# Optimization experiments

Hardware: AMD Instinct MI355X
Metric: run time of the kernel (lower is better)

Reference implementation:

```python
import jax, jax.numpy as jnp
import numpy as np

H = 16       # num_heads
FD = 16      # feature_dim
HD = 64      # head_dim = hidden // num_kv_heads
EPS = 1e-5   # attention normalization eps
LN_EPS = 1e-5


def setup_inputs() -> dict:
    key = jax.random.key(0)
    ks = jax.random.split(key, 5)
    b, l, hid = 2, 2048, 1024
    x = jax.random.normal(ks[0], (b, l, hid), dtype=jnp.float32)
    Wq = jax.random.normal(ks[1], (H * FD, hid), dtype=jnp.float32) * 0.02
    Wk = jax.random.normal(ks[2], (H * FD, hid), dtype=jnp.float32) * 0.02
    Wv = jax.random.normal(ks[3], (hid, hid), dtype=jnp.float32) * 0.02
    Wo = jax.random.normal(ks[4], (hid, hid), dtype=jnp.float32) * 0.02
    gamma = jnp.ones((FD,), dtype=jnp.float32)
    beta = jnp.zeros((FD,), dtype=jnp.float32)
    return {"x": x, "Wq": Wq, "Wk": Wk, "Wv": Wv, "Wo": Wo, "gamma": gamma, "beta": beta}


def _feature_map(t, gamma, beta):
    # RebasedFeatureMap without flatten: layer_norm (no affine) -> *gamma + beta
    mu = jnp.mean(t, axis=-1, keepdims=True)
    var = jnp.mean(jnp.square(t - mu), axis=-1, keepdims=True)
    t = (t - mu) * jax.lax.rsqrt(var + LN_EPS)
    return t * gamma + beta


def reference(x, Wq, Wk, Wv, Wo, gamma, beta):
    b, l, hid = x.shape
    # projections -> (b, h, l, d)
    q = (x @ Wq.T).reshape(b, l, H, FD).transpose(0, 2, 1, 3)
    k = (x @ Wk.T).reshape(b, l, H, FD).transpose(0, 2, 1, 3)
    v = (x @ Wv.T).reshape(b, l, H, HD).transpose(0, 2, 1, 3)
    q = _feature_map(q, gamma, beta) * (FD ** -0.5)  # use_scale=True in parallel_rebased
    k = _feature_map(k, gamma, beta)
    # phi(q).phi(k) with squared feature map == (q.k)^2
    s = jnp.square(jnp.einsum('bhid,bhjd->bhij', q, k))
    mask = jnp.tril(jnp.ones((l, l), dtype=bool))  # causal
    s = jnp.where(mask, s, jnp.float32(0))
    o = jnp.einsum('bhij,bhjd->bhid', s, v)
    z = jnp.sum(s, axis=-1, keepdims=True) + EPS    # use_normalize=True
    o = o / z
    o = o.transpose(0, 2, 1, 3).reshape(b, l, H * HD)
    return o @ Wo.T
```

## Files before the change

### kernel.cpp

```cpp
#include <hip/hip_runtime.h>
#include <cstddef>
#include <cstdint>


typedef __attribute__((ext_vector_type(8)))  __bf16 bf16x8;
typedef __attribute__((ext_vector_type(4)))  __bf16 bf16x4;
typedef __attribute__((ext_vector_type(4)))  float  f32x4;
typedef __attribute__((ext_vector_type(8)))  unsigned short ushort8;
typedef __attribute__((ext_vector_type(4)))  unsigned short ushort4v;

__device__ __forceinline__ unsigned short f2b(float f) {
    union { float f; unsigned u; } v; v.f = f;
    unsigned r = v.u + 0x7FFFu + ((v.u >> 16) & 1u);
    return (unsigned short)(r >> 16);
}
__device__ __forceinline__ float b2f(unsigned short b) {
    union { unsigned u; float f; } v; v.u = ((unsigned)b) << 16;
    return v.f;
}

typedef const __attribute__((address_space(1))) void* gas_ptr;
typedef __attribute__((address_space(3))) void* las_ptr;

__device__ __forceinline__ void gload_lds16(const unsigned short* g, unsigned short* l) {
    __builtin_amdgcn_global_load_lds((gas_ptr)g, (las_ptr)l, 16, 0, 0);
}

template <int BM, int BN, int OUTMODE>
__global__ __launch_bounds__(256) void gemm_mfma(const unsigned short* __restrict__ A,
                                                 const unsigned short* __restrict__ W,
                                                 void* __restrict__ Cout,
                                                 int M, int N, int K) {
    constexpr int BK = 64;
    constexpr int MF = BM / 32;
    constexpr int NF = BN / 32;
    __shared__ __align__(16) unsigned short As[BM * BK];
    __shared__ __align__(16) unsigned short Bs[BN * BK];

    const int t = threadIdx.x;
    const int wid = t >> 6, lane = t & 63;
    const int m0 = blockIdx.x * BM, n0 = blockIdx.y * BN;
    const int wrow = (wid >> 1) * (BM / 2);
    const int wcol = (wid & 1) * (BN / 2);
    const int lr = lane & 15, lk = (lane >> 4) * 8;

    f32x4 acc[MF][NF];
#pragma unroll
    for (int m = 0; m < MF; ++m)
#pragma unroll
        for (int n = 0; n < NF; ++n) acc[m][n] = (f32x4){0.f, 0.f, 0.f, 0.f};

    const unsigned short* Ag = A + (size_t)m0 * K;
    const unsigned short* Wg = W + (size_t)n0 * K;

    for (int k0 = 0; k0 < K; k0 += BK) {
        __syncthreads();
#pragma unroll
        for (int i = 0; i < BM / 32; ++i) {
            const int e = (i * 256 + wid * 64 + lane) * 8;
            gload_lds16(Ag + (size_t)(e >> 6) * K + k0 + (e & 63),
                        As + (size_t)(i * 256 + wid * 64) * 8);
        }
#pragma unroll
        for (int i = 0; i < BN / 32; ++i) {
            const int e = (i * 256 + wid * 64 + lane) * 8;
            gload_lds16(Wg + (size_t)(e >> 6) * K + k0 + (e & 63),
                        Bs + (size_t)(i * 256 + wid * 64) * 8);
        }
        __syncthreads();

#pragma unroll
        for (int kk = 0; kk < BK; kk += 32) {
            bf16x8 af[MF], bf[NF];
#pragma unroll
            for (int m = 0; m < MF; ++m)
                af[m] = *(const bf16x8*)&As[(wrow + m * 16 + lr) * BK + kk + lk];
#pragma unroll
            for (int n = 0; n < NF; ++n)
                bf[n] = *(const bf16x8*)&Bs[(wcol + n * 16 + lr) * BK + kk + lk];
#pragma unroll
            for (int m = 0; m < MF; ++m)
#pragma unroll
                for (int n = 0; n < NF; ++n)
                    acc[m][n] = __builtin_amdgcn_mfma_f32_16x16x32_bf16(af[m], bf[n], acc[m][n], 0, 0, 0);
        }
    }

    const int orow0 = m0 + wrow + (lane >> 4) * 4;
    const int ocol0 = n0 + wcol + lr;
#pragma unroll
    for (int m = 0; m < MF; ++m)
#pragma unroll
        for (int n = 0; n < NF; ++n) {
            if (OUTMODE == 2) {
                const int nc = ocol0 + n * 16;
                const int mrow = orow0 + m * 16;
                unsigned short* dst = (unsigned short*)Cout
                    + (size_t)((mrow >> 11) * 16 + (nc >> 6)) * (64 * 2048)
                    + (size_t)(nc & 63) * 2048 + (mrow & 2047);
                ushort4v pv;
#pragma unroll
                for (int i = 0; i < 4; ++i) pv[i] = f2b(acc[m][n][i]);
                *(ushort4v*)dst = pv;
            } else {
#pragma unroll
                for (int i = 0; i < 4; ++i) {
                    const size_t idx = (size_t)(orow0 + m * 16 + i) * N + ocol0 + n * 16;
                    if (OUTMODE == 1) ((unsigned short*)Cout)[idx] = f2b(acc[m][n][i]);
                    else              ((float*)Cout)[idx] = acc[m][n][i];
                }
            }
        }
}

__global__ __launch_bounds__(256) void gemm_split(const unsigned short* __restrict__ Ah,
                                                  const unsigned short* __restrict__ Al,
                                                  const unsigned short* __restrict__ Wh,
                                                  const unsigned short* __restrict__ Wl,
                                                  float* __restrict__ C,
                                                  int M, int N, int K) {
    constexpr int BM = 64, BN = 64, BK = 64;
    constexpr int MF = 2, NF = 2;
    __shared__ __align__(16) unsigned short Ahs[BM * BK];
    __shared__ __align__(16) unsigned short Als[BM * BK];
    __shared__ __align__(16) unsigned short Bhs[BN * BK];
    __shared__ __align__(16) unsigned short Bls[BN * BK];

    const int t = threadIdx.x;
    const int wid = t >> 6, lane = t & 63;
    const int m0 = blockIdx.x * BM, n0 = blockIdx.y * BN;
    const int wrow = (wid >> 1) * 32;
    const int wcol = (wid & 1) * 32;
    const int lr = lane & 15, lk = (lane >> 4) * 8;

    f32x4 acc[MF][NF];
#pragma unroll
    for (int m = 0; m < MF; ++m)
#pragma unroll
        for (int n = 0; n < NF; ++n) acc[m][n] = (f32x4){0.f, 0.f, 0.f, 0.f};

    const unsigned short* Ahg = Ah + (size_t)m0 * K;
    const unsigned short* Alg = Al + (size_t)m0 * K;
    const unsigned short* Whg = Wh + (size_t)n0 * K;
    const unsigned short* Wlg = Wl + (size_t)n0 * K;

    for (int k0 = 0; k0 < K; k0 += BK) {
        __syncthreads();
#pragma unroll
        for (int i = 0; i < BM / 32; ++i) {
            const int e = (i * 256 + wid * 64 + lane) * 8;
            const size_t go = (size_t)(e >> 6) * K + k0 + (e & 63);
            const size_t lo = (size_t)(i * 256 + wid * 64) * 8;
            gload_lds16(Ahg + go, Ahs + lo);
            gload_lds16(Alg + go, Als + lo);
            gload_lds16(Whg + go, Bhs + lo);
            gload_lds16(Wlg + go, Bls + lo);
        }
        __syncthreads();

#pragma unroll
        for (int kk = 0; kk < BK; kk += 32) {
            bf16x8 afh[MF], afl[MF], bfh[NF], bfl[NF];
#pragma unroll
            for (int m = 0; m < MF; ++m) {
                afh[m] = *(const bf16x8*)&Ahs[(wrow + m * 16 + lr) * BK + kk + lk];
                afl[m] = *(const bf16x8*)&Als[(wrow + m * 16 + lr) * BK + kk + lk];
            }
#pragma unroll
            for (int n = 0; n < NF; ++n) {
                bfh[n] = *(const bf16x8*)&Bhs[(wcol + n * 16 + lr) * BK + kk + lk];
                bfl[n] = *(const bf16x8*)&Bls[(wcol + n * 16 + lr) * BK + kk + lk];
            }
#pragma unroll
            for (int m = 0; m < MF; ++m)
#pragma unroll
                for (int n = 0; n < NF; ++n) {
                    acc[m][n] = __builtin_amdgcn_mfma_f32_16x16x32_bf16(afh[m], bfh[n], acc[m][n], 0, 0, 0);
                    acc[m][n] = __builtin_amdgcn_mfma_f32_16x16x32_bf16(afh[m], bfl[n], acc[m][n], 0, 0, 0);
                    acc[m][n] = __builtin_amdgcn_mfma_f32_16x16x32_bf16(afl[m], bfh[n], acc[m][n], 0, 0, 0);
                }
        }
    }

    const int orow0 = m0 + wrow + (lane >> 4) * 4;
    const int ocol0 = n0 + wcol + lr;
#pragma unroll
    for (int m = 0; m < MF; ++m)
#pragma unroll
        for (int n = 0; n < NF; ++n)
#pragma unroll
            for (int i = 0; i < 4; ++i)
                C[(size_t)(orow0 + m * 16 + i) * N + ocol0 + n * 16] = acc[m][n][i];
}

__global__ __launch_bounds__(256) void cast_bf16(const float* __restrict__ in,
                                                 unsigned short* __restrict__ out, int n) {
    const int i = (blockIdx.x * 256 + threadIdx.x) * 8;
    if (i >= n) return;
    float4 a = *(const float4*)(in + i);
    float4 b = *(const float4*)(in + i + 4);
    ushort8 o;
    o[0] = f2b(a.x); o[1] = f2b(a.y); o[2] = f2b(a.z); o[3] = f2b(a.w);
    o[4] = f2b(b.x); o[5] = f2b(b.y); o[6] = f2b(b.z); o[7] = f2b(b.w);
    *(ushort8*)(out + i) = o;
}

__global__ __launch_bounds__(256) void cast_split(const float* __restrict__ in,
                                                  unsigned short* __restrict__ hi,
                                                  unsigned short* __restrict__ lo, int n) {
    const int i = (blockIdx.x * 256 + threadIdx.x) * 8;
    if (i >= n) return;
    float4 a = *(const float4*)(in + i);
    float4 b = *(const float4*)(in + i + 4);
    float xv[8] = {a.x, a.y, a.z, a.w, b.x, b.y, b.z, b.w};
    ushort8 oh, ol;
#pragma unroll
    for (int e = 0; e < 8; ++e) {
        const unsigned short h = f2b(xv[e]);
        oh[e] = h;
        ol[e] = f2b(xv[e] - b2f(h));
    }
    *(ushort8*)(hi + i) = oh;
    *(ushort8*)(lo + i) = ol;
}

__global__ __launch_bounds__(256) void ln_featuremap(const float* __restrict__ qk,
                                                     const float* __restrict__ gamma,
                                                     const float* __restrict__ beta,
                                                     unsigned short* __restrict__ qhl,
                                                     unsigned short* __restrict__ khl) {
    const int gid = blockIdx.x * 256 + threadIdx.x;
    const int idx = gid & 31;
    const int m = gid >> 5;
    const int b = m >> 11, l = m & 2047;
    const int h = idx & 15;
    const float scale = (idx < 16) ? 0.25f : 1.0f;
    const float* p = qk + (size_t)gid * 16;

    float xv[16];
    float4 v0 = *(const float4*)(p + 0);
    float4 v1 = *(const float4*)(p + 4);
    float4 v2 = *(const float4*)(p + 8);
    float4 v3 = *(const float4*)(p + 12);
    xv[0]=v0.x; xv[1]=v0.y; xv[2]=v0.z; xv[3]=v0.w;
    xv[4]=v1.x; xv[5]=v1.y; xv[6]=v1.z; xv[7]=v1.w;
    xv[8]=v2.x; xv[9]=v2.y; xv[10]=v2.z; xv[11]=v2.w;
    xv[12]=v3.x; xv[13]=v3.y; xv[14]=v3.z; xv[15]=v3.w;

    float mu = 0.f;
#pragma unroll
    for (int f = 0; f < 16; ++f) mu += xv[f];
    mu *= 0.0625f;
    float var = 0.f;
#pragma unroll
    for (int f = 0; f < 16; ++f) { float d = xv[f] - mu; var = fmaf(d, d, var); }
    var *= 0.0625f;
    const float rs = rsqrtf(var + 1e-5f);

    ushort8 hi0, hi1, lo0, lo1;
#pragma unroll
    for (int f = 0; f < 16; ++f) {
        const float v = ((xv[f] - mu) * rs * gamma[f] + beta[f]) * scale;
        const unsigned short hb = f2b(v);
        const unsigned short lb = f2b(v - b2f(hb));
        if (f < 8) { hi0[f] = hb; lo0[f] = lb; }
        else       { hi1[f - 8] = hb; lo1[f - 8] = lb; }
    }
    unsigned short* dst = ((idx < 16) ? qhl : khl)
        + ((size_t)(b * 16 + h) * 2048 + l) * 32;
    *(ushort8*)(dst + 0)  = hi0;
    *(ushort8*)(dst + 8)  = hi1;
    *(ushort8*)(dst + 16) = lo0;
    *(ushort8*)(dst + 24) = lo1;
}

__global__ __launch_bounds__(256) void rebased_attn(const unsigned short* __restrict__ qhl_g,
                                                    const unsigned short* __restrict__ khl_g,
                                                    const unsigned short* __restrict__ vT,
                                                    unsigned short* __restrict__ o) {
    const int bh = blockIdx.y;
    const int bb = bh >> 4;
    const int t = threadIdx.x;
    const int wid = t >> 6, lane = t & 63;
    const int fr = lane & 15;
    const int fg = lane >> 4;

    __shared__ __align__(16) unsigned short qhl[4 * 64 * 8];
    __shared__ __align__(16) unsigned short khl[2][4 * 64 * 8];
    __shared__ __align__(16) unsigned short vsl[2][8 * 64 * 8];
    __shared__ __align__(16) __bf16 P[64][72];

    const unsigned short* qg  = qhl_g + (size_t)bh * 2048 * 32;
    const unsigned short* kg  = khl_g + (size_t)bh * 2048 * 32;
    const unsigned short* vbh = vT + (size_t)bh * 64 * 2048;
    unsigned short*       obh = o  + (size_t)bb * 2048 * 1024 + (bh & 15) * 64;

    const bf16x8 z8 = {(__bf16)0.f,(__bf16)0.f,(__bf16)0.f,(__bf16)0.f,
                       (__bf16)0.f,(__bf16)0.f,(__bf16)0.f,(__bf16)0.f};
    const f32x4 zc = (f32x4){0.f, 0.f, 0.f, 0.f};

    for (int pass = 0; pass < 2; ++pass) {
        const int qt = pass ? (31 - (int)blockIdx.x) : (int)blockIdx.x;
        const int qbase = qt << 6;

        __syncthreads();
        gload_lds16(qg + (size_t)(qbase + lane) * 32 + wid * 8, qhl + wid * 512);
        gload_lds16(kg + (size_t)lane * 32 + wid * 8, &khl[0][wid * 512]);
        gload_lds16(vbh + (size_t)lane * 2048 + (2 * wid) * 8, &vsl[0][(2 * wid) * 512]);
        gload_lds16(vbh + (size_t)lane * 2048 + (2 * wid + 1) * 8, &vsl[0][(2 * wid + 1) * 512]);
        __syncthreads();

        const bf16x8 bq1 = *(const bf16x8*)&qhl[(((fg & 1)    ) * 64 + 16 * wid + fr) * 8];
        const bf16x8 bq2 = *(const bf16x8*)&qhl[(((fg & 1) + 2) * 64 + 16 * wid + fr) * 8];

        f32x4 oacc[4];
#pragma unroll
        for (int n = 0; n < 4; ++n) oacc[n] = zc;
        float zlane = 0.f;

        int cur = 0;
        for (int kt = 0; kt <= qt; ++kt) {
            if (kt < qt) {
                const int nb = cur ^ 1;
                gload_lds16(kg + (size_t)(((kt + 1) << 6) + lane) * 32 + wid * 8,
                            &khl[nb][wid * 512]);
                gload_lds16(vbh + (size_t)lane * 2048 + ((kt + 1) << 6) + (2 * wid) * 8,
                            &vsl[nb][(2 * wid) * 512]);
                gload_lds16(vbh + (size_t)lane * 2048 + ((kt + 1) << 6) + (2 * wid + 1) * 8,
                            &vsl[nb][(2 * wid + 1) * 512]);
            }

#pragma unroll
            for (int nrow = 0; nrow < 4; ++nrow) {
                const bf16x8 ak  = *(const bf16x8*)&khl[cur][(fg * 64 + nrow * 16 + fr) * 8];
                const bf16x8 ak2 = (fg < 2) ? ak : z8;
                f32x4 s = __builtin_amdgcn_mfma_f32_16x16x32_bf16(ak2, bq2, zc, 0, 0, 0);
                s = __builtin_amdgcn_mfma_f32_16x16x32_bf16(ak, bq1, s, 0, 0, 0);

                float s2[4];
                if (kt == qt) {
                    const int qr = 16 * wid + fr;
                    const int kc = nrow * 16 + fg * 4;
#pragma unroll
                    for (int reg = 0; reg < 4; ++reg) {
                        float x = s[reg];
                        float y = x * x;
                        s2[reg] = (kc + reg <= qr) ? y : 0.f;
                        zlane += s2[reg];
                    }
                } else {
#pragma unroll
                    for (int reg = 0; reg < 4; ++reg) {
                        float x = s[reg];
                        s2[reg] = x * x;
                        zlane += s2[reg];
                    }
                }
                bf16x4 pv = {(__bf16)s2[0], (__bf16)s2[1], (__bf16)s2[2], (__bf16)s2[3]};
                *(bf16x4*)&P[16 * wid + fr][nrow * 16 + fg * 4] = pv;
            }

            const bf16x8 a0 = *(const bf16x8*)&P[16 * wid + fr][fg * 8];
            const bf16x8 a1 = *(const bf16x8*)&P[16 * wid + fr][32 + fg * 8];
#pragma unroll
            for (int nt = 0; nt < 4; ++nt) {
                const bf16x8 b0 = *(const bf16x8*)&vsl[cur][((fg    ) * 64 + nt * 16 + fr) * 8];
                const bf16x8 b1 = *(const bf16x8*)&vsl[cur][((fg + 4) * 64 + nt * 16 + fr) * 8];
                oacc[nt] = __builtin_amdgcn_mfma_f32_16x16x32_bf16(a0, b0, oacc[nt], 0, 0, 0);
                oacc[nt] = __builtin_amdgcn_mfma_f32_16x16x32_bf16(a1, b1, oacc[nt], 0, 0, 0);
            }

            asm volatile("s_waitcnt vmcnt(0)" ::: "memory");
            __builtin_amdgcn_s_barrier();
            cur ^= 1;
        }

        float z = zlane;
        z += __shfl_xor(z, 16);
        z += __shfl_xor(z, 32);
        const float zinv = 1.f / (z + 1e-5f);

#pragma unroll
        for (int reg = 0; reg < 4; ++reg) {
            const float r = __shfl(zinv, fg * 4 + reg);
            const size_t gro = (size_t)(qbase + 16 * wid + fg * 4 + reg) * 1024;
#pragma unroll
            for (int nt = 0; nt < 4; ++nt)
                obh[gro + nt * 16 + fr] = f2b(oacc[nt][reg] * r);
        }
    }
}

extern "C" void kernel_launch(void* const* d_in, const int* in_sizes, int n_in,
                              void* d_out, int out_size, void* d_ws, size_t ws_size,
                              hipStream_t stream) {
    const float* x     = (const float*)d_in[0];
    const float* Wq    = (const float*)d_in[1];
    const float* Wk    = (const float*)d_in[2];
    const float* Wv    = (const float*)d_in[3];
    const float* Wo    = (const float*)d_in[4];
    const float* gamma = (const float*)d_in[5];
    const float* beta  = (const float*)d_in[6];
    float* out = (float*)d_out;
    (void)in_sizes; (void)n_in; (void)out_size; (void)ws_size;

    char* w = (char*)d_ws;
    float*          qk_raw = (float*)w;
    unsigned short* vTb    = (unsigned short*)(w + (8u  << 20));
    unsigned short* ob     = (unsigned short*)(w + (16u << 20));
    unsigned short* xh     = (unsigned short*)(w + (24u << 20));
    unsigned short* xl     = (unsigned short*)(w + (32u << 20));
    unsigned short* qhl_g  = (unsigned short*)(w + (24u << 20));
    unsigned short* khl_g  = (unsigned short*)(w + (28u << 20));
    unsigned short* wqkh   = (unsigned short*)(w + (40u << 20));
    unsigned short* wqkl   = (unsigned short*)(w + (41u << 20));
    unsigned short* wvb    = (unsigned short*)(w + (42u << 20));
    unsigned short* wob    = (unsigned short*)(w + (44u << 20));

    cast_split<<<2048, 256, 0, stream>>>(x,  xh, xl, 4096 * 1024);
    cast_split<<<128,  256, 0, stream>>>(Wq, wqkh, wqkl, 256 * 1024);
    cast_split<<<128,  256, 0, stream>>>(Wk, wqkh + 256 * 1024, wqkl + 256 * 1024, 256 * 1024);
    cast_bf16 <<<512,  256, 0, stream>>>(Wv, wvb, 1024 * 1024);
    cast_bf16 <<<512,  256, 0, stream>>>(Wo, wob, 1024 * 1024);

    gemm_split<<<dim3(64, 8), 256, 0, stream>>>(xh, xl, wqkh, wqkl, qk_raw, 4096, 512, 1024);
    gemm_mfma<64, 128, 2><<<dim3(64, 8), 256, 0, stream>>>(xh, wvb, vTb, 4096, 1024, 1024);
    ln_featuremap<<<512, 256, 0, stream>>>(qk_raw, gamma, beta, qhl_g, khl_g);
    rebased_attn<<<dim3(16, 32), 256, 0, stream>>>(qhl_g, khl_g, vTb, ob);
    gemm_mfma<64, 128, 0><<<dim3(64, 8), 256, 0, stream>>>(ob, wob, out, 4096, 1024, 1024);
}
```

Before: 125.3 us.

## Use one query tile per block with triple-buffered KV prefetch and smaller GEMM tiles

The attention kernel no longer pairs query tiles i and 31-i inside one block. It launches 32 query tiles per head, each handled by its own block, and loads the Q fragments straight from global memory into registers. K/V staging goes from double to triple buffering, with a partial vmcnt wait so two tiles can be in flight while one is computed. The V-projection and output GEMMs switch to 64x64 tiles with twice the grid. These changes aim to raise occupancy and overlap memory latency. In exchange the causal work per block becomes unbalanced and each block uses more LDS.

```diff
diff --git a/kernel.cpp b/kernel.cpp
--- a/kernel.cpp
+++ b/kernel.cpp
@@ -284,10 +284,11 @@
     const int wid = t >> 6, lane = t & 63;
     const int fr = lane & 15;
     const int fg = lane >> 4;
-
-    __shared__ __align__(16) unsigned short qhl[4 * 64 * 8];
-    __shared__ __align__(16) unsigned short khl[2][4 * 64 * 8];
-    __shared__ __align__(16) unsigned short vsl[2][8 * 64 * 8];
+    const int qt = blockIdx.x;
+    const int qbase = qt << 6;
+
+    __shared__ __align__(16) unsigned short khl[3][4 * 64 * 8];
+    __shared__ __align__(16) unsigned short vsl[3][8 * 64 * 8];
     __shared__ __align__(16) __bf16 P[64][72];
 
     const unsigned short* qg  = qhl_g + (size_t)bh * 2048 * 32;
@@ -299,95 +300,93 @@
                        (__bf16)0.f,(__bf16)0.f,(__bf16)0.f,(__bf16)0.f};
     const f32x4 zc = (f32x4){0.f, 0.f, 0.f, 0.f};
 
-    for (int pass = 0; pass < 2; ++pass) {
-        const int qt = pass ? (31 - (int)blockIdx.x) : (int)blockIdx.x;
-        const int qbase = qt << 6;
-
-        __syncthreads();
-        gload_lds16(qg + (size_t)(qbase + lane) * 32 + wid * 8, qhl + wid * 512);
-        gload_lds16(kg + (size_t)lane * 32 + wid * 8, &khl[0][wid * 512]);
-        gload_lds16(vbh + (size_t)lane * 2048 + (2 * wid) * 8, &vsl[0][(2 * wid) * 512]);
-        gload_lds16(vbh + (size_t)lane * 2048 + (2 * wid + 1) * 8, &vsl[0][(2 * wid + 1) * 512]);
-        __syncthreads();
-
-        const bf16x8 bq1 = *(const bf16x8*)&qhl[(((fg & 1)    ) * 64 + 16 * wid + fr) * 8];
-        const bf16x8 bq2 = *(const bf16x8*)&qhl[(((fg & 1) + 2) * 64 + 16 * wid + fr) * 8];
-
-        f32x4 oacc[4];
-#pragma unroll
-        for (int n = 0; n < 4; ++n) oacc[n] = zc;
-        float zlane = 0.f;
-
-        int cur = 0;
-        for (int kt = 0; kt <= qt; ++kt) {
-            if (kt < qt) {
-                const int nb = cur ^ 1;
-                gload_lds16(kg + (size_t)(((kt + 1) << 6) + lane) * 32 + wid * 8,
-                            &khl[nb][wid * 512]);
-                gload_lds16(vbh + (size_t)lane * 2048 + ((kt + 1) << 6) + (2 * wid) * 8,
-                            &vsl[nb][(2 * wid) * 512]);
-                gload_lds16(vbh + (size_t)lane * 2048 + ((kt + 1) << 6) + (2 * wid + 1) * 8,
-                            &vsl[nb][(2 * wid + 1) * 512]);
+    const unsigned short* qrow = qg + (size_t)(qbase + 16 * wid + fr) * 32;
+    const bf16x8 bq1 = *(const bf16x8*)&qrow[(fg & 1) * 8];
+    const bf16x8 bq2 = *(const bf16x8*)&qrow[((fg & 1) + 2) * 8];
+
+#define STAGE_KV(kt_, buf_)                                                          \
+    do {                                                                             \
+        gload_lds16(kg + ((size_t)((kt_) << 6) + lane) * 32 + wid * 8,               \
+                    &khl[buf_][wid * 512]);                                          \
+        gload_lds16(vbh + (size_t)lane * 2048 + ((kt_) << 6) + (2 * wid) * 8,        \
+                    &vsl[buf_][(2 * wid) * 512]);                                    \
+        gload_lds16(vbh + (size_t)lane * 2048 + ((kt_) << 6) + (2 * wid + 1) * 8,    \
+                    &vsl[buf_][(2 * wid + 1) * 512]);                                \
+    } while (0)
+
+    STAGE_KV(0, 0);
+    if (qt >= 1) STAGE_KV(1, 1);
+    asm volatile("s_waitcnt vmcnt(0)" ::: "memory");
+    __syncthreads();
+
+    f32x4 oacc[4];
+#pragma unroll
+    for (int n = 0; n < 4; ++n) oacc[n] = zc;
+    float zlane = 0.f;
+
+    for (int kt = 0; kt <= qt; ++kt) {
+        const int cur = kt % 3;
+        if (kt + 2 <= qt) STAGE_KV(kt + 2, (kt + 2) % 3);
+
+#pragma unroll
+        for (int nrow = 0; nrow < 4; ++nrow) {
+            const bf16x8 ak  = *(const bf16x8*)&khl[cur][(fg * 64 + nrow * 16 + fr) * 8];
+            const bf16x8 ak2 = (fg < 2) ? ak : z8;
+            f32x4 s = __builtin_amdgcn_mfma_f32_16x16x32_bf16(ak2, bq2, zc, 0, 0, 0);
+            s = __builtin_amdgcn_mfma_f32_16x16x32_bf16(ak, bq1, s, 0, 0, 0);
+
+            float s2[4];
+            if (kt == qt) {
+                const int qr = 16 * wid + fr;
+                const int kc = nrow * 16 + fg * 4;
+#pragma unroll
+                for (int reg = 0; reg < 4; ++reg) {
+                    float x = s[reg];
+                    float y = x * x;
+                    s2[reg] = (kc + reg <= qr) ? y : 0.f;
+                    zlane += s2[reg];
+                }
+            } else {
+#pragma unroll
+                for (int reg = 0; reg < 4; ++reg) {
+                    float x = s[reg];
+                    s2[reg] = x * x;
+                    zlane += s2[reg];
+                }
             }
-
-#pragma unroll
-            for (int nrow = 0; nrow < 4; ++nrow) {
-                const bf16x8 ak  = *(const bf16x8*)&khl[cur][(fg * 64 + nrow * 16 + fr) * 8];
-                const bf16x8 ak2 = (fg < 2) ? ak : z8;
-                f32x4 s = __builtin_amdgcn_mfma_f32_16x16x32_bf16(ak2, bq2, zc, 0, 0, 0);
-                s = __builtin_amdgcn_mfma_f32_16x16x32_bf16(ak, bq1, s, 0, 0, 0);
-
-                float s2[4];
-                if (kt == qt) {
-                    const int qr = 16 * wid + fr;
-                    const int kc = nrow * 16 + fg * 4;
-#pragma unroll
-                    for (int reg = 0; reg < 4; ++reg) {
-                        float x = s[reg];
-                        float y = x * x;
-                        s2[reg] = (kc + reg <= qr) ? y : 0.f;
-                        zlane += s2[reg];
-                    }
-                } else {
-#pragma unroll
-                    for (int reg = 0; reg < 4; ++reg) {
-                        float x = s[reg];
-                        s2[reg] = x * x;
-                        zlane += s2[reg];
-                    }
-                }
-                bf16x4 pv = {(__bf16)s2[0], (__bf16)s2[1], (__bf16)s2[2], (__bf16)s2[3]};
-                *(bf16x4*)&P[16 * wid + fr][nrow * 16 + fg * 4] = pv;
-            }
-
-            const bf16x8 a0 = *(const bf16x8*)&P[16 * wid + fr][fg * 8];
-            const bf16x8 a1 = *(const bf16x8*)&P[16 * wid + fr][32 + fg * 8];
-#pragma unroll
-            for (int nt = 0; nt < 4; ++nt) {
-                const bf16x8 b0 = *(const bf16x8*)&vsl[cur][((fg    ) * 64 + nt * 16 + fr) * 8];
-                const bf16x8 b1 = *(const bf16x8*)&vsl[cur][((fg + 4) * 64 + nt * 16 + fr) * 8];
-                oacc[nt] = __builtin_amdgcn_mfma_f32_16x16x32_bf16(a0, b0, oacc[nt], 0, 0, 0);
-                oacc[nt] = __builtin_amdgcn_mfma_f32_16x16x32_bf16(a1, b1, oacc[nt], 0, 0, 0);
-            }
-
-            asm volatile("s_waitcnt vmcnt(0)" ::: "memory");
-            __builtin_amdgcn_s_barrier();
-            cur ^= 1;
-        }
-
-        float z = zlane;
-        z += __shfl_xor(z, 16);
-        z += __shfl_xor(z, 32);
-        const float zinv = 1.f / (z + 1e-5f);
-
-#pragma unroll
-        for (int reg = 0; reg < 4; ++reg) {
-            const float r = __shfl(zinv, fg * 4 + reg);
-            const size_t gro = (size_t)(qbase + 16 * wid + fg * 4 + reg) * 1024;
-#pragma unroll
-            for (int nt = 0; nt < 4; ++nt)
-                obh[gro + nt * 16 + fr] = f2b(oacc[nt][reg] * r);
-        }
+            bf16x4 pv = {(__bf16)s2[0], (__bf16)s2[1], (__bf16)s2[2], (__bf16)s2[3]};
+            *(bf16x4*)&P[16 * wid + fr][nrow * 16 + fg * 4] = pv;
+        }
+
+        const bf16x8 a0 = *(const bf16x8*)&P[16 * wid + fr][fg * 8];
+        const bf16x8 a1 = *(const bf16x8*)&P[16 * wid + fr][32 + fg * 8];
+#pragma unroll
+        for (int nt = 0; nt < 4; ++nt) {
+            const bf16x8 b0 = *(const bf16x8*)&vsl[cur][((fg    ) * 64 + nt * 16 + fr) * 8];
+            const bf16x8 b1 = *(const bf16x8*)&vsl[cur][((fg + 4) * 64 + nt * 16 + fr) * 8];
+            oacc[nt] = __builtin_amdgcn_mfma_f32_16x16x32_bf16(a0, b0, oacc[nt], 0, 0, 0);
+            oacc[nt] = __builtin_amdgcn_mfma_f32_16x16x32_bf16(a1, b1, oacc[nt], 0, 0, 0);
+        }
+
+        if (kt + 2 <= qt) asm volatile("s_waitcnt vmcnt(3)" ::: "memory");
+        else              asm volatile("s_waitcnt vmcnt(0)" ::: "memory");
+        __builtin_amdgcn_s_barrier();
+        __builtin_amdgcn_sched_barrier(0);
+    }
+#undef STAGE_KV
+
+    float z = zlane;
+    z += __shfl_xor(z, 16);
+    z += __shfl_xor(z, 32);
+    const float zinv = 1.f / (z + 1e-5f);
+
+#pragma unroll
+    for (int reg = 0; reg < 4; ++reg) {
+        const float r = __shfl(zinv, fg * 4 + reg);
+        const size_t gro = (size_t)(qbase + 16 * wid + fg * 4 + reg) * 1024;
+#pragma unroll
+        for (int nt = 0; nt < 4; ++nt)
+            obh[gro + nt * 16 + fr] = f2b(oacc[nt][reg] * r);
     }
 }
 
@@ -424,8 +423,8 @@
     cast_bf16 <<<512,  256, 0, stream>>>(Wo, wob, 1024 * 1024);
 
     gemm_split<<<dim3(64, 8), 256, 0, stream>>>(xh, xl, wqkh, wqkl, qk_raw, 4096, 512, 1024);
-    gemm_mfma<64, 128, 2><<<dim3(64, 8), 256, 0, stream>>>(xh, wvb, vTb, 4096, 1024, 1024);
+    gemm_mfma<64, 64, 2><<<dim3(64, 16), 256, 0, stream>>>(xh, wvb, vTb, 4096, 1024, 1024);
     ln_featuremap<<<512, 256, 0, stream>>>(qk_raw, gamma, beta, qhl_g, khl_g);
-    rebased_attn<<<dim3(16, 32), 256, 0, stream>>>(qhl_g, khl_g, vTb, ob);
-    gemm_mfma<64, 128, 0><<<dim3(64, 8), 256, 0, stream>>>(ob, wob, out, 4096, 1024, 1024);
-}
+    rebased_attn<<<dim3(32, 32), 256, 0, stream>>>(qhl_g, khl_g, vTb, ob);
+    gemm_mfma<64, 64, 0><<<dim3(64, 16), 256, 0, stream>>>(ob, wob, out, 4096, 1024, 1024);
+}
```

Result: slower. 163.2 us (+30.2%).
